# Kernel optimization log

Hardware: AMD Instinct MI355X
Metric: run time of the kernel (lower is better)

Reference implementation:

```python
import jax, jax.numpy as jnp
import numpy as np

B = 50000      # batch of graphs
NOBJ = 7       # tangram pieces per graph
HID = 64
EMB = 32
SIGMA = 25.0   # VE-SDE sigma for marginal_prob_std


def _lin_init(k, fin, fout):
    kw, kb = jax.random.split(k)
    s = 1.0 / np.sqrt(fin)
    w = jax.random.uniform(kw, (fin, fout), minval=-s, maxval=s, dtype=jnp.float32)
    b = jax.random.uniform(kb, (fout,), minval=-s, maxval=s, dtype=jnp.float32)
    return w, b


def setup_inputs() -> dict:
    key = jax.random.key(0)
    ks = jax.random.split(key, 16)
    N = B * NOBJ
    omega = jax.random.normal(ks[0], (N, 3), dtype=jnp.float32)
    t = jax.random.uniform(ks[1], (B, 1), minval=1e-3, maxval=1.0, dtype=jnp.float32)
    # fully-connected edges (no self loops) per graph, offset by graph index
    a, b = np.meshgrid(np.arange(NOBJ), np.arange(NOBJ), indexing='ij')
    m = a != b
    src0, dst0 = a[m], b[m]                       # (42,)
    offs = (np.arange(B) * NOBJ)[:, None]         # (B,1)
    src = (src0[None, :] + offs).reshape(-1)
    dst = (dst0[None, :] + offs).reshape(-1)
    edge_index = jnp.asarray(np.stack([src, dst]), dtype=jnp.int32)  # (2, B*42)
    W_fourier = jax.random.normal(ks[2], (EMB // 2,), dtype=jnp.float32) * 30.0
    wi1, bi1 = _lin_init(ks[3], 3, HID)
    wi2, bi2 = _lin_init(ks[4], HID, HID)
    wt, bt = _lin_init(ks[5], EMB, EMB)
    w1a, b1a = _lin_init(ks[6], HID * 2, HID)
    w1b, b1b = _lin_init(ks[7], HID, HID)
    w2a, b2a = _lin_init(ks[8], (HID + EMB) * 2, HID)
    w2b, b2b = _lin_init(ks[9], HID, HID)
    w3a, b3a = _lin_init(ks[10], (HID + EMB) * 2, HID)
    w3b, b3b = _lin_init(ks[11], HID, 3)
    return dict(omega=omega, edge_index=edge_index, t=t, num_objs=NOBJ,
                W_fourier=W_fourier,
                wi1=wi1, bi1=bi1, wi2=wi2, bi2=bi2, wt=wt, bt=bt,
                w1a=w1a, b1a=b1a, w1b=w1b, b1b=b1b,
                w2a=w2a, b2a=b2a, w2b=w2b, b2b=b2b,
                w3a=w3a, b3a=b3a, w3b=w3b, b3b=b3b)


def _mlp(x, wa, ba, wb, bb):
    return jax.nn.relu(x @ wa + ba) @ wb + bb


def reference(omega, edge_index, t, num_objs, W_fourier,
              wi1, bi1, wi2, bi2, wt, bt,
              w1a, b1a, w1b, b1b, w2a, b2a, w2b, b2b, w3a, b3a, w3b, b3b):
    N = omega.shape[0]
    src, dst = edge_index[0], edge_index[1]

    def edge_conv(x, wa, ba, wb, bb):
        # EdgeConv: msg = mlp([x_i, x_j - x_i]); max-aggregate at target i
        xi = x[dst]
        msg = _mlp(jnp.concatenate([xi, x[src] - xi], axis=-1), wa, ba, wb, bb)
        return jax.ops.segment_max(msg, dst, num_segments=N)

    init_feature = _mlp(omega, wi1, bi1, wi2, bi2)          # (N, HID)
    # Gaussian Fourier time embedding -> ReLU -> Linear -> ReLU
    proj = t[:, 0][:, None] * W_fourier[None, :] * (2.0 * jnp.pi)   # (B, EMB/2)
    emb = jnp.concatenate([jnp.sin(proj), jnp.cos(proj)], axis=-1)  # (B, EMB)
    xs = jax.nn.relu(jax.nn.relu(emb) @ wt + bt)                    # (B, EMB)
    # torch: xs.repeat(1, num_objs, 1).view(B*num_objs, -1) == tile whole block
    x_sigma = jnp.tile(xs, (num_objs, 1))                           # (N, EMB)

    x = jax.nn.relu(edge_conv(init_feature, w1a, b1a, w1b, b1b))
    x = jnp.concatenate([x, x_sigma], axis=-1)
    x = jax.nn.relu(edge_conv(x, w2a, b2a, w2b, b2b))
    x = jnp.concatenate([x, x_sigma], axis=-1)
    x = edge_conv(x, w3a, b3a, w3b, b3b)                            # (N, 3)

    # torch: t.repeat(1, num_objs).view(B*num_objs, -1) == repeat_interleave
    t_r = jnp.repeat(t, num_objs, axis=0)                           # (N, 1)
    std = jnp.sqrt((SIGMA ** (2.0 * t_r) - 1.0) / (2.0 * jnp.log(SIGMA)))
    return x / (std + 1e-7)
```

## Files before the change

kernel.cpp:

```cpp
#include <hip/hip_runtime.h>


#define NB 50000

typedef unsigned short u16;
typedef short short8 __attribute__((ext_vector_type(8)));
typedef float f32x4 __attribute__((ext_vector_type(4)));

#define OFF_I  0
#define OFF_1A 8192
#define OFF_2A 24576
#define OFF_3A 49152
#define OFF_1B 73728
#define OFF_2B 81920
#define OFF_WT 90112
#define OFF_3B 92160

#define XSTR 208
#define XLO  3328
#define HSTR 144
#define HLO  2304
#define SSTR 264
#define WREG 10880

__device__ __forceinline__ float b2f(u16 u) {
    return __uint_as_float(((unsigned int)u) << 16);
}
__device__ __forceinline__ u16 f2b(float f) {
    unsigned int u = __float_as_uint(f);
    u += 0x7FFFu + ((u >> 16) & 1u);
    return (u16)(u >> 16);
}
__device__ __forceinline__ float bcast(float v, int l) {
    return __uint_as_float(__builtin_amdgcn_readlane(__float_as_uint(v), l));
}

__global__ __launch_bounds__(128) void pack_kernel(
    const float* __restrict__ wi2, const float* __restrict__ w1a,
    const float* __restrict__ w2a, const float* __restrict__ w3a,
    const float* __restrict__ w1b, const float* __restrict__ w2b,
    const float* __restrict__ wt,  const float* __restrict__ w3b,
    u16* __restrict__ ws)
{
    int blk = blockIdx.x;
    int half = threadIdx.x >> 6;
    int lane = threadIdx.x & 63;
    if (blk < 88) {
        const float* src; int NT, qoff, obase, frag;
        if (blk < 8)       { src = wi2; NT = 4; qoff = 0;  obase = OFF_I;  frag = blk;      }
        else if (blk < 24) { src = w1a; NT = 8; qoff = 64; obase = OFF_1A; frag = blk - 8;  }
        else if (blk < 48) { src = w2a; NT = 8; qoff = 96; obase = OFF_2A; frag = blk - 24; }
        else if (blk < 72) { src = w3a; NT = 8; qoff = 96; obase = OFF_3A; frag = blk - 48; }
        else if (blk < 80) { src = w1b; NT = 4; qoff = 0;  obase = OFF_1B; frag = blk - 72; }
        else               { src = w2b; NT = 4; qoff = 0;  obase = OFF_2B; frag = blk - 80; }
        int kt = frag / NT, nt = frag % NT;
        int k0 = kt * 32 + (lane >> 4) * 8;
        int n  = nt * 16 + (lane & 15);
        u16* dst = ws + obase + frag * 1024 + half * 512 + lane * 8;
#pragma unroll
        for (int j = 0; j < 8; ++j) {
            int k = k0 + j;
            int idx = (n < 64) ? (k * 64 + n) : ((qoff + k) * 64 + (n - 64));
            float v = src[idx];
            u16 hi = f2b(v);
            dst[j] = (half == 0) ? hi : f2b(v - b2f(hi));
        }
    } else if (blk < 90) {
        int frag = blk - 88;
        int k0 = (lane >> 4) * 8;
        int n  = frag * 16 + (lane & 15);
        u16* dst = ws + OFF_WT + frag * 1024 + half * 512 + lane * 8;
#pragma unroll
        for (int j = 0; j < 8; ++j) {
            float v = wt[(k0 + j) * 32 + n];
            u16 hi = f2b(v);
            dst[j] = (half == 0) ? hi : f2b(v - b2f(hi));
        }
    } else {
        int frag = blk - 90;
        int k0 = frag * 32 + (lane >> 4) * 8;
        int n  = lane & 15;
        u16* dst = ws + OFF_3B + frag * 1024 + half * 512 + lane * 8;
#pragma unroll
        for (int j = 0; j < 8; ++j) {
            float v = (n < 3) ? w3b[(k0 + j) * 3 + n] : 0.f;
            u16 hi = f2b(v);
            dst[j] = (half == 0) ? hi : f2b(v - b2f(hi));
        }
    }
}

__device__ __forceinline__ f32x4 mfma3(short8 ah, short8 al, short8 bh, short8 bl, f32x4 acc) {
    acc = __builtin_amdgcn_mfma_f32_16x16x32_bf16(ah, bh, acc, 0, 0, 0);
    acc = __builtin_amdgcn_mfma_f32_16x16x32_bf16(ah, bl, acc, 0, 0, 0);
    acc = __builtin_amdgcn_mfma_f32_16x16x32_bf16(al, bh, acc, 0, 0, 0);
    return acc;
}

#define ROW(k) ((k) < 7 ? (k) : (k) + 1)

__device__ __forceinline__ void writeX64_14(char* XH, int L, const float* v) {
#pragma unroll
    for (int k = 0; k < 14; ++k) {
        int r = ROW(k);
        u16 hi = f2b(v[k]);
        *(u16*)(XH + r * XSTR + L * 2) = hi;
        *(u16*)(XH + XLO + r * XSTR + L * 2) = f2b(v[k] - b2f(hi));
    }
}
__device__ __forceinline__ void writeXS14(char* XH, int L, const float* xs) {
    int cc = L & 31;
    int off = (L < 32) ? 0 : XLO;
#pragma unroll
    for (int k = 0; k < 14; ++k) {
        float v = xs[k];
        u16 hi = f2b(v);
        u16 w = (L < 32) ? hi : f2b(v - b2f(hi));
        *(u16*)(XH + off + ROW(k) * XSTR + 128 + cc * 2) = w;
    }
}
template<int KT>
__device__ __forceinline__ void loadA(const char* XH, int L, short8* Ah, short8* Al) {
#pragma unroll
    for (int kt = 0; kt < KT; ++kt) {
        Ah[kt] = *(const short8*)(XH + (L & 15) * XSTR + kt * 64 + (L >> 4) * 16);
        Al[kt] = *(const short8*)(XH + XLO + (L & 15) * XSTR + kt * 64 + (L >> 4) * 16);
    }
}
template<int KT, int NT>
__device__ __forceinline__ void lin_pass(const u16* __restrict__ ws, int off, int nt0,
                                         const short8* Ah, const short8* Al,
                                         char* Sb, int L) {
#pragma unroll
    for (int ntc = 0; ntc < 4; ++ntc) {
        f32x4 acc = {0.f, 0.f, 0.f, 0.f};
#pragma unroll
        for (int kt = 0; kt < KT; ++kt) {
            int f = kt * NT + nt0 + ntc;
            short8 bh = *(const short8*)(ws + off + f * 1024 + L * 8);
            short8 bl = *(const short8*)(ws + off + f * 1024 + 512 + L * 8);
            acc = mfma3(Ah[kt], Al[kt], bh, bl, acc);
        }
#pragma unroll
        for (int rr = 0; rr < 4; ++rr)
            *(float*)(Sb + ((L >> 4) * 4 + rr) * SSTR + ntc * 64 + (L & 15) * 4) = acc[rr];
    }
}
__device__ __forceinline__ void readS14(const char* Sb, int L, float* o) {
#pragma unroll
    for (int k = 0; k < 14; ++k) o[k] = *(const float*)(Sb + ROW(k) * SSTR + L * 4);
}
__device__ __forceinline__ void stageH2(char* XH, int c, const float* pp, const float* qq, int L) {
#pragma unroll
    for (int r = 0; r < 16; ++r) {
        int e = c * 16 + r;
        if (e < 84) {
            int gb = (e >= 42) ? 1 : 0;
            int el = e - gb * 42;
            int i = el / 6, jj = el - i * 6;
            int j = jj + (jj >= i);
            float hv = fmaxf(pp[gb * 7 + i] + qq[gb * 7 + j], 0.f);
            u16 hi = f2b(hv);
            *(u16*)(XH + r * HSTR + L * 2) = hi;
            *(u16*)(XH + HLO + r * HSTR + L * 2) = f2b(hv - b2f(hi));
        }
    }
}
__device__ __forceinline__ void loadAH(const char* XH, int L,
                                       short8& Ah0, short8& Ah1, short8& Al0, short8& Al1) {
    Ah0 = *(const short8*)(XH + (L & 15) * HSTR + (L >> 4) * 16);
    Ah1 = *(const short8*)(XH + (L & 15) * HSTR + 64 + (L >> 4) * 16);
    Al0 = *(const short8*)(XH + HLO + (L & 15) * HSTR + (L >> 4) * 16);
    Al1 = *(const short8*)(XH + HLO + (L & 15) * HSTR + 64 + (L >> 4) * 16);
}

__device__ __forceinline__ void edgeconv2(const u16* __restrict__ ws, int offB,
                                          char* XH, char* Sb,
                                          const float* pp, const float* qq,
                                          float vb, int L, float* xout) {
    short8 Bh[8], Bl[8];
#pragma unroll
    for (int f = 0; f < 8; ++f) {
        Bh[f] = *(const short8*)(ws + offB + f * 1024 + L * 8);
        Bl[f] = *(const short8*)(ws + offB + f * 1024 + 512 + L * 8);
    }
    float mx[14];
#pragma unroll
    for (int k = 0; k < 14; ++k) mx[k] = -3.0e38f;
#pragma unroll
    for (int c = 0; c < 6; ++c) {
        stageH2(XH, c, pp, qq, L);
        short8 Ah0, Ah1, Al0, Al1;
        loadAH(XH, L, Ah0, Ah1, Al0, Al1);
#pragma unroll
        for (int nt = 0; nt < 4; ++nt) {
            f32x4 acc = {0.f, 0.f, 0.f, 0.f};
            acc = mfma3(Ah0, Al0, Bh[nt], Bl[nt], acc);
            acc = mfma3(Ah1, Al1, Bh[4 + nt], Bl[4 + nt], acc);
#pragma unroll
            for (int rr = 0; rr < 4; ++rr)
                *(float*)(Sb + ((L >> 4) * 4 + rr) * SSTR + nt * 64 + (L & 15) * 4) = acc[rr];
        }
#pragma unroll
        for (int r = 0; r < 16; ++r) {
            int e = c * 16 + r;
            if (e < 84) {
                int gb = (e >= 42) ? 1 : 0;
                int i = (e - gb * 42) / 6;
                float sv = *(const float*)(Sb + r * SSTR + L * 4);
                mx[gb * 7 + i] = fmaxf(mx[gb * 7 + i], sv);
            }
        }
    }
#pragma unroll
    for (int k = 0; k < 14; ++k) xout[k] = fmaxf(mx[k] + vb, 0.f);
}

__global__ __launch_bounds__(256) void gnn_kernel(
    const float* __restrict__ omega, const float* __restrict__ tt, const float* __restrict__ Wf,
    const float* __restrict__ wi1, const float* __restrict__ bi1, const float* __restrict__ bi2,
    const float* __restrict__ bt,
    const float* __restrict__ b1a, const float* __restrict__ b1b,
    const float* __restrict__ b2a, const float* __restrict__ b2b,
    const float* __restrict__ b3a, const float* __restrict__ b3b,
    const u16* __restrict__ ws, float* __restrict__ out)
{
    __shared__ __align__(16) char smem[4 * WREG];
    const int L   = threadIdx.x & 63;
    const int wav = threadIdx.x >> 6;
    const int p   = blockIdx.x * 4 + wav;
    const int g0  = p * 2;
    const int base0 = g0 * 7;
    char* XH = smem + wav * WREG;
    char* Sb = XH + 6656;

    float omv = (L < 42) ? omega[base0 * 3 + L] : 0.f;
    float vwi10 = wi1[L], vwi11 = wi1[64 + L], vwi12 = wi1[128 + L];
    float vbi1 = bi1[L];
    float h1[14];
#pragma unroll
    for (int k = 0; k < 14; ++k) {
        float a0 = bcast(omv, 3 * k), a1 = bcast(omv, 3 * k + 1), a2 = bcast(omv, 3 * k + 2);
        h1[k] = fmaxf(fmaf(a0, vwi10, fmaf(a1, vwi11, fmaf(a2, vwi12, vbi1))), 0.f);
    }

    float xs[14];
    {
        int cc = L & 31;
        float vwf = Wf[cc & 15] * 6.283185307179586f;
        int off = (L < 32) ? 0 : XLO;
        int tb = base0 - (base0 / NB) * NB;
#pragma unroll
        for (int k = 0; k < 14; ++k) {
            int ti = tb + k; if (ti >= NB) ti -= NB;
            float pj = tt[ti] * vwf;
            float remb = fmaxf((cc < 16) ? sinf(pj) : cosf(pj), 0.f);
            u16 hi = f2b(remb);
            u16 w = (L < 32) ? hi : f2b(remb - b2f(hi));
            *(u16*)(XH + off + ROW(k) * XSTR + cc * 2) = w;
        }
        short8 Eh = *(const short8*)(XH + (L & 15) * XSTR + (L >> 4) * 16);
        short8 El = *(const short8*)(XH + XLO + (L & 15) * XSTR + (L >> 4) * 16);
#pragma unroll
        for (int nt = 0; nt < 2; ++nt) {
            short8 bh = *(const short8*)(ws + OFF_WT + nt * 1024 + L * 8);
            short8 bl = *(const short8*)(ws + OFF_WT + nt * 1024 + 512 + L * 8);
            f32x4 acc = {0.f, 0.f, 0.f, 0.f};
            acc = mfma3(Eh, El, bh, bl, acc);
#pragma unroll
            for (int rr = 0; rr < 4; ++rr)
                *(float*)(Sb + ((L >> 4) * 4 + rr) * SSTR + nt * 64 + (L & 15) * 4) = acc[rr];
        }
        float vbt = bt[cc];
#pragma unroll
        for (int k = 0; k < 14; ++k)
            xs[k] = fmaxf(*(const float*)(Sb + ROW(k) * SSTR + cc * 4) + vbt, 0.f);
    }

    short8 Ah[3], Al[3];
    float xh[14], pp[14], qq[14];

    writeX64_14(XH, L, h1);
    loadA<2>(XH, L, Ah, Al);
    lin_pass<2, 4>(ws, OFF_I, 0, Ah, Al, Sb, L);
    readS14(Sb, L, xh);
    float vbi2 = bi2[L];
#pragma unroll
    for (int k = 0; k < 14; ++k) xh[k] += vbi2;

    writeX64_14(XH, L, xh);
    loadA<2>(XH, L, Ah, Al);
    lin_pass<2, 8>(ws, OFF_1A, 0, Ah, Al, Sb, L);
    readS14(Sb, L, pp);
    lin_pass<2, 8>(ws, OFF_1A, 4, Ah, Al, Sb, L);
    readS14(Sb, L, qq);
    float vb1a = b1a[L];
#pragma unroll
    for (int k = 0; k < 14; ++k) pp[k] = pp[k] + vb1a - qq[k];
    edgeconv2(ws, OFF_1B, XH, Sb, pp, qq, b1b[L], L, xh);

    writeX64_14(XH, L, xh);
    writeXS14(XH, L, xs);
    loadA<3>(XH, L, Ah, Al);
    lin_pass<3, 8>(ws, OFF_2A, 0, Ah, Al, Sb, L);
    readS14(Sb, L, pp);
    lin_pass<3, 8>(ws, OFF_2A, 4, Ah, Al, Sb, L);
    readS14(Sb, L, qq);
    float vb2a = b2a[L];
#pragma unroll
    for (int k = 0; k < 14; ++k) pp[k] = pp[k] + vb2a - qq[k];
    edgeconv2(ws, OFF_2B, XH, Sb, pp, qq, b2b[L], L, xh);

    writeX64_14(XH, L, xh);
    writeXS14(XH, L, xs);
    loadA<3>(XH, L, Ah, Al);
    lin_pass<3, 8>(ws, OFF_3A, 0, Ah, Al, Sb, L);
    readS14(Sb, L, pp);
    lin_pass<3, 8>(ws, OFF_3A, 4, Ah, Al, Sb, L);
    readS14(Sb, L, qq);
    float vb3a = b3a[L];
#pragma unroll
    for (int k = 0; k < 14; ++k) pp[k] = pp[k] + vb3a - qq[k];

    {
        short8 B0h = *(const short8*)(ws + OFF_3B + L * 8);
        short8 B0l = *(const short8*)(ws + OFF_3B + 512 + L * 8);
        short8 B1h = *(const short8*)(ws + OFF_3B + 1024 + L * 8);
        short8 B1l = *(const short8*)(ws + OFF_3B + 1536 + L * 8);
#pragma unroll
        for (int c = 0; c < 6; ++c) {
            stageH2(XH, c, pp, qq, L);
            short8 Ah0, Ah1, Al0, Al1;
            loadAH(XH, L, Ah0, Ah1, Al0, Al1);
            f32x4 acc = {0.f, 0.f, 0.f, 0.f};
            acc = mfma3(Ah0, Al0, B0h, B0l, acc);
            acc = mfma3(Ah1, Al1, B1h, B1l, acc);
            if ((L & 15) < 3) {
#pragma unroll
                for (int rr = 0; rr < 4; ++rr)
                    *(float*)(Sb + (c * 16 + (L >> 4) * 4 + rr) * 16 + (L & 15) * 4) = acc[rr];
            }
        }
        if (L < 42) {
            int gb = (L >= 21) ? 1 : 0;
            int ll = L - gb * 21;
            int i = ll / 3, col = ll - i * 3;
            int e0 = gb * 42 + i * 6;
            float m = -3.0e38f;
#pragma unroll
            for (int e6 = 0; e6 < 6; ++e6)
                m = fmaxf(m, *(const float*)(Sb + (e0 + e6) * 16 + col * 4));
            m += b3b[col];
            float tg = tt[g0 + gb];
            float stdv = sqrtf((exp2f(tg * 9.287712379549448f) - 1.0f) * 0.15533740282828987f);
            out[base0 * 3 + L] = m / (stdv + 1e-7f);
        }
    }
}

extern "C" void kernel_launch(void* const* d_in, const int* in_sizes, int n_in,
                              void* d_out, int out_size, void* d_ws, size_t ws_size,
                              hipStream_t stream) {
    const float* omega = (const float*)d_in[0];
    const float* tt  = (const float*)d_in[2];
    const float* Wf  = (const float*)d_in[4];
    const float* wi1 = (const float*)d_in[5];
    const float* bi1 = (const float*)d_in[6];
    const float* wi2 = (const float*)d_in[7];
    const float* bi2 = (const float*)d_in[8];
    const float* wt  = (const float*)d_in[9];
    const float* bt  = (const float*)d_in[10];
    const float* w1a = (const float*)d_in[11];
    const float* b1a = (const float*)d_in[12];
    const float* w1b = (const float*)d_in[13];
    const float* b1b = (const float*)d_in[14];
    const float* w2a = (const float*)d_in[15];
    const float* b2a = (const float*)d_in[16];
    const float* w2b = (const float*)d_in[17];
    const float* b2b = (const float*)d_in[18];
    const float* w3a = (const float*)d_in[19];
    const float* b3a = (const float*)d_in[20];
    const float* w3b = (const float*)d_in[21];
    const float* b3b = (const float*)d_in[22];
    u16* ws = (u16*)d_ws;

    pack_kernel<<<dim3(92), dim3(128), 0, stream>>>(wi2, w1a, w2a, w3a, w1b, w2b, wt, w3b, ws);
    gnn_kernel<<<dim3(6250), dim3(256), 0, stream>>>(
        omega, tt, Wf, wi1, bi1, bi2, bt,
        b1a, b1b, b2a, b2b, b3a, b3b, ws, (float*)d_out);
}
```

Measured before the change: 493.4 us.

## Cut register pressure by staging x_sigma once in LDS and streaming edge weights

The time embedding x_sigma is now converted to bf16 hi/lo once and kept in a dedicated LDS region, instead of living in 14 registers and being rewritten before every layer. The edge-conv B weights are loaded per tile inside the loop rather than held as 16 short8 registers, and the edge-conv output is written straight to LDS. Blocks shrink to 2 waves with a doubled grid. The goal is lower VGPR use and higher occupancy, at the cost of repeated global/L2 weight loads inside the inner loop.

New measurement: 487.3 us. Within noise of the previous version (-1.2%).

```diff
diff --git a/kernel.cpp b/kernel.cpp
--- a/kernel.cpp
+++ b/kernel.cpp
@@ -16,12 +16,12 @@
 #define OFF_WT 90112
 #define OFF_3B 92160
 
-#define XSTR 208
-#define XLO  3328
 #define HSTR 144
 #define HLO  2304
+#define XS2S 72
+#define XS2LO 1152
 #define SSTR 264
-#define WREG 10880
+#define WREG 11136
 
 __device__ __forceinline__ float b2f(u16 u) {
     return __uint_as_float(((unsigned int)u) << 16);
@@ -99,32 +99,27 @@
 
 #define ROW(k) ((k) < 7 ? (k) : (k) + 1)
 
-__device__ __forceinline__ void writeX64_14(char* XH, int L, const float* v) {
+__device__ __forceinline__ void writeX64_14(char* W, int L, const float* v) {
 #pragma unroll
     for (int k = 0; k < 14; ++k) {
         int r = ROW(k);
         u16 hi = f2b(v[k]);
-        *(u16*)(XH + r * XSTR + L * 2) = hi;
-        *(u16*)(XH + XLO + r * XSTR + L * 2) = f2b(v[k] - b2f(hi));
-    }
-}
-__device__ __forceinline__ void writeXS14(char* XH, int L, const float* xs) {
-    int cc = L & 31;
-    int off = (L < 32) ? 0 : XLO;
-#pragma unroll
-    for (int k = 0; k < 14; ++k) {
-        float v = xs[k];
-        u16 hi = f2b(v);
-        u16 w = (L < 32) ? hi : f2b(v - b2f(hi));
-        *(u16*)(XH + off + ROW(k) * XSTR + 128 + cc * 2) = w;
+        *(u16*)(W + r * HSTR + L * 2) = hi;
+        *(u16*)(W + HLO + r * HSTR + L * 2) = f2b(v[k] - b2f(hi));
     }
 }
 template<int KT>
-__device__ __forceinline__ void loadA(const char* XH, int L, short8* Ah, short8* Al) {
+__device__ __forceinline__ void loadA(const char* W, const char* XS2, int L,
+                                      short8* Ah, short8* Al) {
 #pragma unroll
     for (int kt = 0; kt < KT; ++kt) {
-        Ah[kt] = *(const short8*)(XH + (L & 15) * XSTR + kt * 64 + (L >> 4) * 16);
-        Al[kt] = *(const short8*)(XH + XLO + (L & 15) * XSTR + kt * 64 + (L >> 4) * 16);
+        if (kt < 2) {
+            Ah[kt] = *(const short8*)(W + (L & 15) * HSTR + kt * 64 + (L >> 4) * 16);
+            Al[kt] = *(const short8*)(W + HLO + (L & 15) * HSTR + kt * 64 + (L >> 4) * 16);
+        } else {
+            Ah[kt] = *(const short8*)(XS2 + (L & 15) * XS2S + (L >> 4) * 16);
+            Al[kt] = *(const short8*)(XS2 + XS2LO + (L & 15) * XS2S + (L >> 4) * 16);
+        }
     }
 }
 template<int KT, int NT>
@@ -150,7 +145,7 @@
 #pragma unroll
     for (int k = 0; k < 14; ++k) o[k] = *(const float*)(Sb + ROW(k) * SSTR + L * 4);
 }
-__device__ __forceinline__ void stageH2(char* XH, int c, const float* pp, const float* qq, int L) {
+__device__ __forceinline__ void stageH2(char* W, int c, const float* pp, const float* qq, int L) {
 #pragma unroll
     for (int r = 0; r < 16; ++r) {
         int e = c * 16 + r;
@@ -161,42 +156,40 @@
             int j = jj + (jj >= i);
             float hv = fmaxf(pp[gb * 7 + i] + qq[gb * 7 + j], 0.f);
             u16 hi = f2b(hv);
-            *(u16*)(XH + r * HSTR + L * 2) = hi;
-            *(u16*)(XH + HLO + r * HSTR + L * 2) = f2b(hv - b2f(hi));
-        }
-    }
-}
-__device__ __forceinline__ void loadAH(const char* XH, int L,
+            *(u16*)(W + r * HSTR + L * 2) = hi;
+            *(u16*)(W + HLO + r * HSTR + L * 2) = f2b(hv - b2f(hi));
+        }
+    }
+}
+__device__ __forceinline__ void loadAH(const char* W, int L,
                                        short8& Ah0, short8& Ah1, short8& Al0, short8& Al1) {
-    Ah0 = *(const short8*)(XH + (L & 15) * HSTR + (L >> 4) * 16);
-    Ah1 = *(const short8*)(XH + (L & 15) * HSTR + 64 + (L >> 4) * 16);
-    Al0 = *(const short8*)(XH + HLO + (L & 15) * HSTR + (L >> 4) * 16);
-    Al1 = *(const short8*)(XH + HLO + (L & 15) * HSTR + 64 + (L >> 4) * 16);
+    Ah0 = *(const short8*)(W + (L & 15) * HSTR + (L >> 4) * 16);
+    Ah1 = *(const short8*)(W + (L & 15) * HSTR + 64 + (L >> 4) * 16);
+    Al0 = *(const short8*)(W + HLO + (L & 15) * HSTR + (L >> 4) * 16);
+    Al1 = *(const short8*)(W + HLO + (L & 15) * HSTR + 64 + (L >> 4) * 16);
 }
 
 __device__ __forceinline__ void edgeconv2(const u16* __restrict__ ws, int offB,
-                                          char* XH, char* Sb,
+                                          char* W, char* Sb,
                                           const float* pp, const float* qq,
-                                          float vb, int L, float* xout) {
-    short8 Bh[8], Bl[8];
-#pragma unroll
-    for (int f = 0; f < 8; ++f) {
-        Bh[f] = *(const short8*)(ws + offB + f * 1024 + L * 8);
-        Bl[f] = *(const short8*)(ws + offB + f * 1024 + 512 + L * 8);
-    }
+                                          float vb, int L) {
     float mx[14];
 #pragma unroll
     for (int k = 0; k < 14; ++k) mx[k] = -3.0e38f;
 #pragma unroll
     for (int c = 0; c < 6; ++c) {
-        stageH2(XH, c, pp, qq, L);
+        stageH2(W, c, pp, qq, L);
         short8 Ah0, Ah1, Al0, Al1;
-        loadAH(XH, L, Ah0, Ah1, Al0, Al1);
+        loadAH(W, L, Ah0, Ah1, Al0, Al1);
 #pragma unroll
         for (int nt = 0; nt < 4; ++nt) {
+            short8 bh0 = *(const short8*)(ws + offB + nt * 1024 + L * 8);
+            short8 bl0 = *(const short8*)(ws + offB + nt * 1024 + 512 + L * 8);
+            short8 bh1 = *(const short8*)(ws + offB + (4 + nt) * 1024 + L * 8);
+            short8 bl1 = *(const short8*)(ws + offB + (4 + nt) * 1024 + 512 + L * 8);
             f32x4 acc = {0.f, 0.f, 0.f, 0.f};
-            acc = mfma3(Ah0, Al0, Bh[nt], Bl[nt], acc);
-            acc = mfma3(Ah1, Al1, Bh[4 + nt], Bl[4 + nt], acc);
+            acc = mfma3(Ah0, Al0, bh0, bl0, acc);
+            acc = mfma3(Ah1, Al1, bh1, bl1, acc);
 #pragma unroll
             for (int rr = 0; rr < 4; ++rr)
                 *(float*)(Sb + ((L >> 4) * 4 + rr) * SSTR + nt * 64 + (L & 15) * 4) = acc[rr];
@@ -212,11 +205,13 @@
             }
         }
     }
-#pragma unroll
-    for (int k = 0; k < 14; ++k) xout[k] = fmaxf(mx[k] + vb, 0.f);
-}
-
-__global__ __launch_bounds__(256) void gnn_kernel(
+    float xo[14];
+#pragma unroll
+    for (int k = 0; k < 14; ++k) xo[k] = fmaxf(mx[k] + vb, 0.f);
+    writeX64_14(W, L, xo);
+}
+
+__global__ __launch_bounds__(128) void gnn_kernel(
     const float* __restrict__ omega, const float* __restrict__ tt, const float* __restrict__ Wf,
     const float* __restrict__ wi1, const float* __restrict__ bi1, const float* __restrict__ bi2,
     const float* __restrict__ bt,
@@ -225,14 +220,15 @@
     const float* __restrict__ b3a, const float* __restrict__ b3b,
     const u16* __restrict__ ws, float* __restrict__ out)
 {
-    __shared__ __align__(16) char smem[4 * WREG];
+    __shared__ __align__(16) char smem[2 * WREG];
     const int L   = threadIdx.x & 63;
     const int wav = threadIdx.x >> 6;
-    const int p   = blockIdx.x * 4 + wav;
+    const int p   = blockIdx.x * 2 + wav;
     const int g0  = p * 2;
     const int base0 = g0 * 7;
-    char* XH = smem + wav * WREG;
-    char* Sb = XH + 6656;
+    char* W   = smem + wav * WREG;
+    char* XS2 = W + 4608;
+    char* Sb  = W + 6912;
 
     float omv = (L < 42) ? omega[base0 * 3 + L] : 0.f;
     float vwi10 = wi1[L], vwi11 = wi1[64 + L], vwi12 = wi1[128 + L];
@@ -244,11 +240,9 @@
         h1[k] = fmaxf(fmaf(a0, vwi10, fmaf(a1, vwi11, fmaf(a2, vwi12, vbi1))), 0.f);
     }
 
-    float xs[14];
     {
         int cc = L & 31;
         float vwf = Wf[cc & 15] * 6.283185307179586f;
-        int off = (L < 32) ? 0 : XLO;
         int tb = base0 - (base0 / NB) * NB;
 #pragma unroll
         for (int k = 0; k < 14; ++k) {
@@ -256,11 +250,11 @@
             float pj = tt[ti] * vwf;
             float remb = fmaxf((cc < 16) ? sinf(pj) : cosf(pj), 0.f);
             u16 hi = f2b(remb);
-            u16 w = (L < 32) ? hi : f2b(remb - b2f(hi));
-            *(u16*)(XH + off + ROW(k) * XSTR + cc * 2) = w;
-        }
-        short8 Eh = *(const short8*)(XH + (L & 15) * XSTR + (L >> 4) * 16);
-        short8 El = *(const short8*)(XH + XLO + (L & 15) * XSTR + (L >> 4) * 16);
+            if (L < 32) *(u16*)(W + ROW(k) * HSTR + cc * 2) = hi;
+            else *(u16*)(W + HLO + ROW(k) * HSTR + cc * 2) = f2b(remb - b2f(hi));
+        }
+        short8 Eh = *(const short8*)(W + (L & 15) * HSTR + (L >> 4) * 16);
+        short8 El = *(const short8*)(W + HLO + (L & 15) * HSTR + (L >> 4) * 16);
 #pragma unroll
         for (int nt = 0; nt < 2; ++nt) {
             short8 bh = *(const short8*)(ws + OFF_WT + nt * 1024 + L * 8);
@@ -273,23 +267,30 @@
         }
         float vbt = bt[cc];
 #pragma unroll
-        for (int k = 0; k < 14; ++k)
-            xs[k] = fmaxf(*(const float*)(Sb + ROW(k) * SSTR + cc * 4) + vbt, 0.f);
+        for (int k = 0; k < 14; ++k) {
+            float xv = fmaxf(*(const float*)(Sb + ROW(k) * SSTR + cc * 4) + vbt, 0.f);
+            u16 hi = f2b(xv);
+            if (L < 32) *(u16*)(XS2 + ROW(k) * XS2S + cc * 2) = hi;
+            else *(u16*)(XS2 + XS2LO + ROW(k) * XS2S + cc * 2) = f2b(xv - b2f(hi));
+        }
     }
 
     short8 Ah[3], Al[3];
-    float xh[14], pp[14], qq[14];
-
-    writeX64_14(XH, L, h1);
-    loadA<2>(XH, L, Ah, Al);
+    float pp[14], qq[14];
+
+    writeX64_14(W, L, h1);
+    loadA<2>(W, XS2, L, Ah, Al);
     lin_pass<2, 4>(ws, OFF_I, 0, Ah, Al, Sb, L);
-    readS14(Sb, L, xh);
-    float vbi2 = bi2[L];
-#pragma unroll
-    for (int k = 0; k < 14; ++k) xh[k] += vbi2;
-
-    writeX64_14(XH, L, xh);
-    loadA<2>(XH, L, Ah, Al);
+    {
+        float xh[14];
+        readS14(Sb, L, xh);
+        float vbi2 = bi2[L];
+#pragma unroll
+        for (int k = 0; k < 14; ++k) xh[k] += vbi2;
+        writeX64_14(W, L, xh);
+    }
+
+    loadA<2>(W, XS2, L, Ah, Al);
     lin_pass<2, 8>(ws, OFF_1A, 0, Ah, Al, Sb, L);
     readS14(Sb, L, pp);
     lin_pass<2, 8>(ws, OFF_1A, 4, Ah, Al, Sb, L);
@@ -297,11 +298,9 @@
     float vb1a = b1a[L];
 #pragma unroll
     for (int k = 0; k < 14; ++k) pp[k] = pp[k] + vb1a - qq[k];
-    edgeconv2(ws, OFF_1B, XH, Sb, pp, qq, b1b[L], L, xh);
-
-    writeX64_14(XH, L, xh);
-    writeXS14(XH, L, xs);
-    loadA<3>(XH, L, Ah, Al);
+    edgeconv2(ws, OFF_1B, W, Sb, pp, qq, b1b[L], L);
+
+    loadA<3>(W, XS2, L, Ah, Al);
     lin_pass<3, 8>(ws, OFF_2A, 0, Ah, Al, Sb, L);
     readS14(Sb, L, pp);
     lin_pass<3, 8>(ws, OFF_2A, 4, Ah, Al, Sb, L);
@@ -309,11 +308,9 @@
     float vb2a = b2a[L];
 #pragma unroll
     for (int k = 0; k < 14; ++k) pp[k] = pp[k] + vb2a - qq[k];
-    edgeconv2(ws, OFF_2B, XH, Sb, pp, qq, b2b[L], L, xh);
-
-    writeX64_14(XH, L, xh);
-    writeXS14(XH, L, xs);
-    loadA<3>(XH, L, Ah, Al);
+    edgeconv2(ws, OFF_2B, W, Sb, pp, qq, b2b[L], L);
+
+    loadA<3>(W, XS2, L, Ah, Al);
     lin_pass<3, 8>(ws, OFF_3A, 0, Ah, Al, Sb, L);
     readS14(Sb, L, pp);
     lin_pass<3, 8>(ws, OFF_3A, 4, Ah, Al, Sb, L);
@@ -329,9 +326,9 @@
         short8 B1l = *(const short8*)(ws + OFF_3B + 1536 + L * 8);
 #pragma unroll
         for (int c = 0; c < 6; ++c) {
-            stageH2(XH, c, pp, qq, L);
+            stageH2(W, c, pp, qq, L);
             short8 Ah0, Ah1, Al0, Al1;
-            loadAH(XH, L, Ah0, Ah1, Al0, Al1);
+            loadAH(W, L, Ah0, Ah1, Al0, Al1);
             f32x4 acc = {0.f, 0.f, 0.f, 0.f};
             acc = mfma3(Ah0, Al0, B0h, B0l, acc);
             acc = mfma3(Ah1, Al1, B1h, B1l, acc);
@@ -385,7 +382,7 @@
     u16* ws = (u16*)d_ws;
 
     pack_kernel<<<dim3(92), dim3(128), 0, stream>>>(wi2, w1a, w2a, w3a, w1b, w2b, wt, w3b, ws);
-    gnn_kernel<<<dim3(6250), dim3(256), 0, stream>>>(
+    gnn_kernel<<<dim3(12500), dim3(128), 0, stream>>>(
         omega, tt, Wf, wi1, bi1, bi2, bt,
         b1a, b1b, b2a, b2b, b3a, b3b, ws, (float*)d_out);
 }
```
